# Kernel tuning notes

Measured on AMD Instinct MI355X. Metric: run time of the kernel, lower is better.

Reference implementation:

```python
import jax, jax.numpy as jnp
import numpy as np

N, E, K, IN_C, D = 50000, 800000, 3, 2, 64
RES_LAYERS = 2
EPS = 1e-5


def setup_inputs() -> dict:
    key = jax.random.key(0)
    ks = jax.random.split(key, 12)
    def w(k, shape, scale=0.05):
        return jax.random.normal(k, shape, jnp.float32) * scale
    x = jax.random.normal(ks[0], (N, IN_C), jnp.float32)
    edge_index = jax.random.randint(ks[1], (2, E), 0, N, dtype=jnp.int32)
    edge_attr = jax.random.uniform(ks[2], (E,), jnp.float32)
    # TAGConv params: first conv IN_C->D, then 2*RES_LAYERS + 1 = 5 convs D->D, each with K+1 weight mats
    tag0_w = w(ks[3], (K + 1, IN_C, D))
    tag0_b = jnp.zeros((D,), jnp.float32)
    tag_w = w(ks[4], (5, K + 1, D, D))
    tag_b = jnp.zeros((5, D), jnp.float32)
    # EdgeModel params: Lin(2D+1,D) + 2 residual blocks (Lin,ReLU,Lin)+LN + Lin(D,1)
    We0 = w(ks[5], (2 * D + 1, D)); be0 = jnp.zeros((D,), jnp.float32)
    ln0_g = jnp.ones((D,), jnp.float32); ln0_b = jnp.zeros((D,), jnp.float32)
    Wa = w(ks[6], (2, D, D)); ba = jnp.zeros((2, D), jnp.float32)
    Wb = w(ks[7], (2, D, D)); bb = jnp.zeros((2, D), jnp.float32)
    ln_g = jnp.ones((2, D), jnp.float32); ln_b = jnp.zeros((2, D), jnp.float32)
    Wf = w(ks[8], (D, 1)); bf = jnp.zeros((1,), jnp.float32)
    return dict(x=x, edge_index=edge_index, edge_attr=edge_attr,
                tag0_w=tag0_w, tag0_b=tag0_b, tag_w=tag_w, tag_b=tag_b,
                We0=We0, be0=be0, ln0_g=ln0_g, ln0_b=ln0_b,
                Wa=Wa, ba=ba, Wb=Wb, bb=bb, ln_g=ln_g, ln_b=ln_b,
                Wf=Wf, bf=bf)


def _gcn_norm(row, col, ew, n):
    # symmetric GCN normalization without self loops (PyG TAGConv default)
    deg = jnp.zeros((n,), ew.dtype).at[col].add(ew)
    deg_safe = jnp.where(deg > 0, deg, 1.0)
    dinv = jnp.where(deg > 0, jax.lax.rsqrt(deg_safe), 0.0)
    return dinv[row] * ew * dinv[col]


def _tagconv(x, row, col, norm, W, b):
    # out = sum_{k=0..K} (A_norm^k x) @ W[k] + b
    out = x @ W[0]
    h = x
    for k in range(1, K + 1):
        h = jnp.zeros(h.shape, h.dtype).at[col].add(norm[:, None] * h[row])
        out = out + h @ W[k]
    return out + b


def _inorm(x):
    # PyG InstanceNorm, single graph, affine=False: per-channel stats over nodes
    m = x.mean(0)
    v = x.var(0)
    return (x - m) * jax.lax.rsqrt(v + EPS)


def _lnorm(x, g, b):
    m = x.mean(-1, keepdims=True)
    v = x.var(-1, keepdims=True)
    return (x - m) * jax.lax.rsqrt(v + EPS) * g + b


def _forward(x, edge_index, edge_attr, tag0_w, tag0_b, tag_w, tag_b,
             We0, be0, ln0_g, ln0_b, Wa, ba, Wb, bb, ln_g, ln_b, Wf, bf):
    row, col = edge_index[0], edge_index[1]
    ew = edge_attr.reshape(-1)
    norm = _gcn_norm(row, col, ew, x.shape[0])
    # block 0: TAGConv(IN_C->D) -> InstanceNorm -> (no residual: shape change) -> ReLU
    data = jax.nn.relu(_inorm(_tagconv(x, row, col, norm, tag0_w, tag0_b)))
    # residual blocks: TAGConv -> ReLU -> TAGConv -> InstanceNorm -> +residual -> ReLU
    for i in range(RES_LAYERS):
        h = jax.nn.relu(_tagconv(data, row, col, norm, tag_w[2 * i], tag_b[2 * i]))
        h = _inorm(_tagconv(h, row, col, norm, tag_w[2 * i + 1], tag_b[2 * i + 1]))
        data = jax.nn.relu(h + data)
    # final block: TAGConv -> (no norm) -> +residual -> ReLU
    data = jax.nn.relu(_tagconv(data, row, col, norm, tag_w[4], tag_b[4]) + data)
    # edge model on gathered endpoint features + edge attr
    e = jnp.concatenate([data[row], data[col], ew[:, None]], axis=1)  # [E, 2D+1]
    h = jax.nn.relu(_lnorm(e @ We0 + be0, ln0_g, ln0_b))  # no residual (shape change)
    for j in range(2):
        h2 = jax.nn.relu(h @ Wa[j] + ba[j]) @ Wb[j] + bb[j]
        h = jax.nn.relu(_lnorm(h2, ln_g[j], ln_b[j]) + h)
    out = h @ Wf + bf  # [E, 1]
    out = (out - out.mean()) / out.std(ddof=1)
    return jnp.abs(out)


def reference(x, edge_index, edge_attr, tag0_w, tag0_b, tag_w, tag_b,
              We0, be0, ln0_g, ln0_b, Wa, ba, Wb, bb, ln_g, ln_b, Wf, bf):
    return _forward(x, edge_index, edge_attr, tag0_w, tag0_b, tag_w, tag_b,
                    We0, be0, ln0_g, ln0_b, Wa, ba, Wb, bb, ln_g, ln_b, Wf, bf)
```

## Files before the change

### kernel.cpp

```cpp
#include <hip/hip_runtime.h>

#define NN 50000
#define NE 800000
#define EPSf 1e-5f

typedef _Float16 half8 __attribute__((ext_vector_type(8)));
typedef _Float16 half4v __attribute__((ext_vector_type(4)));
typedef _Float16 half2v __attribute__((ext_vector_type(2)));
typedef float f32x4 __attribute__((ext_vector_type(4)));

#define HA_STRIDE 72
#define WB_STRIDE 72

__global__ void deg_hist_kernel(const int* __restrict__ row, const int* __restrict__ col,
                                const float* __restrict__ ew,
                                float* __restrict__ deg, int* __restrict__ cnt) {
  int e = blockIdx.x * 256 + threadIdx.x;
  if (e >= NE) return;
  int c = col[e];
  unsafeAtomicAdd(&deg[c], ew[e]);
  atomicAdd(&cnt[c], 1);
}

__global__ void dinv_kernel(float* __restrict__ deg) {
  int n = blockIdx.x * 256 + threadIdx.x;
  if (n >= NN) return;
  float d = deg[n];
  deg[n] = d > 0.f ? rsqrtf(d) : 0.f;
}

__global__ void scan1(int* __restrict__ cnt, int* __restrict__ aux) {
  __shared__ int ls[256];
  int t = threadIdx.x, idx = blockIdx.x * 256 + t;
  int v = (idx < NN) ? cnt[idx] : 0;
  ls[t] = v;
  __syncthreads();
  for (int o = 1; o < 256; o <<= 1) {
    int u = (t >= o) ? ls[t - o] : 0;
    __syncthreads();
    ls[t] += u;
    __syncthreads();
  }
  if (idx < NN) cnt[idx] = ls[t] - v;
  if (t == 255) aux[blockIdx.x] = ls[255];
}

__global__ void scan2(int* __restrict__ aux, int nb) {
  __shared__ int ls[256];
  int t = threadIdx.x;
  int v = (t < nb) ? aux[t] : 0;
  ls[t] = v;
  __syncthreads();
  for (int o = 1; o < 256; o <<= 1) {
    int u = (t >= o) ? ls[t - o] : 0;
    __syncthreads();
    ls[t] += u;
    __syncthreads();
  }
  if (t < nb) aux[t] = ls[t] - v;
}

__global__ void scan3(int* __restrict__ cnt, const int* __restrict__ aux) {
  int idx = blockIdx.x * 256 + threadIdx.x;
  if (idx < NN) cnt[idx] += aux[idx >> 8];
}

__global__ void scatter_kernel(const int* __restrict__ row, const int* __restrict__ col,
                               const float* __restrict__ ew, const float* __restrict__ dinv,
                               int* __restrict__ rowptr, int2* __restrict__ pme) {
  int e = blockIdx.x * 256 + threadIdx.x;
  if (e >= NE) return;
  int r = row[e], c = col[e];
  float w = dinv[r] * ew[e] * dinv[c];
  int p = atomicAdd(&rowptr[c], 1);
  pme[p] = make_int2(r, __float_as_int(w));
}

__global__ void cvt_w(const float* __restrict__ We0, const float* __restrict__ Wa,
                      const float* __restrict__ Wb, _Float16* __restrict__ wt) {
  int i = blockIdx.x * 256 + threadIdx.x;
  if (i < 8192) {
    int n = i >> 7, k = i & 127;
    wt[i] = (_Float16)We0[k * 64 + n];
  } else if (i < 16384) {
    int i2 = i - 8192, j = i2 >> 12, n = (i2 >> 6) & 63, k = i2 & 63;
    wt[i] = (_Float16)Wa[j * 4096 + k * 64 + n];
  } else if (i < 24576) {
    int i2 = i - 16384, j = i2 >> 12, n = (i2 >> 6) & 63, k = i2 & 63;
    wt[i] = (_Float16)Wb[j * 4096 + k * 64 + n];
  }
}

__global__ void prop16(const int* __restrict__ rowptr, const int2* __restrict__ pme,
                       const _Float16* __restrict__ h, _Float16* __restrict__ hn) {
  int idx = blockIdx.x * 256 + threadIdx.x;
  if (idx >= NN * 4) return;
  int n = idx >> 2, q = idx & 3;
  int s = n ? rowptr[n - 1] : 0;
  int epos = rowptr[n];
  const _Float16* hq = h + q * 16;
  float a[16];
#pragma unroll
  for (int i = 0; i < 16; i++) a[i] = 0.f;
  int j = s;
  for (; j + 4 <= epos; j += 4) {
    int2 m0 = pme[j], m1 = pme[j + 1], m2 = pme[j + 2], m3 = pme[j + 3];
    const half8* p0 = (const half8*)&hq[(size_t)m0.x * 64];
    const half8* p1 = (const half8*)&hq[(size_t)m1.x * 64];
    const half8* p2 = (const half8*)&hq[(size_t)m2.x * 64];
    const half8* p3 = (const half8*)&hq[(size_t)m3.x * 64];
    half8 u0 = p0[0], u1 = p0[1];
    half8 u2 = p1[0], u3 = p1[1];
    half8 u4 = p2[0], u5 = p2[1];
    half8 u6 = p3[0], u7 = p3[1];
    float w0 = __int_as_float(m0.y), w1 = __int_as_float(m1.y);
    float w2 = __int_as_float(m2.y), w3 = __int_as_float(m3.y);
#pragma unroll
    for (int i = 0; i < 8; i++) {
      a[i]     += w0 * (float)u0[i] + w1 * (float)u2[i] + w2 * (float)u4[i] + w3 * (float)u6[i];
      a[i + 8] += w0 * (float)u1[i] + w1 * (float)u3[i] + w2 * (float)u5[i] + w3 * (float)u7[i];
    }
  }
  for (; j < epos; j++) {
    int2 m = pme[j];
    float w = __int_as_float(m.y);
    const half8* p = (const half8*)&hq[(size_t)m.x * 64];
    half8 u0 = p[0], u1 = p[1];
#pragma unroll
    for (int i = 0; i < 8; i++) { a[i] += w * (float)u0[i]; a[i + 8] += w * (float)u1[i]; }
  }
  half8 o0, o1;
#pragma unroll
  for (int i = 0; i < 8; i++) { o0[i] = (_Float16)a[i]; o1[i] = (_Float16)a[i + 8]; }
  *(half8*)&hn[(size_t)n * 64 + q * 16] = o0;
  *(half8*)&hn[(size_t)n * 64 + q * 16 + 8] = o1;
}

__global__ void prop2_csr(const int* __restrict__ rowptr, const int2* __restrict__ pme,
                          const float* __restrict__ h, float* __restrict__ hn) {
  int n = blockIdx.x * 256 + threadIdx.x;
  if (n >= NN) return;
  int s = n ? rowptr[n - 1] : 0;
  int epos = rowptr[n];
  float a0 = 0.f, a1 = 0.f;
  for (int j = s; j < epos; j++) {
    int2 m = pme[j];
    float w = __int_as_float(m.y);
    a0 += w * h[m.x * 2 + 0];
    a1 += w * h[m.x * 2 + 1];
  }
  hn[n * 2 + 0] = a0;
  hn[n * 2 + 1] = a1;
}

__global__ void __launch_bounds__(128, 4) gemmB_mfma(
    const _Float16* __restrict__ h0, const _Float16* __restrict__ h1,
    const _Float16* __restrict__ h2, const _Float16* __restrict__ h3,
    const float* __restrict__ W,
    float* __restrict__ accG, const float* __restrict__ bias,
    const float* __restrict__ residF, _Float16* __restrict__ out16,
    float* __restrict__ st) {
  __shared__ __align__(16) _Float16 hA[128 * HA_STRIDE];
  __shared__ __align__(16) _Float16 WT[64 * WB_STRIDE];
  const int t = threadIdx.x;
  const int lane = t & 63, wv = t >> 6;
  const int a = lane & 15, g = lane >> 4;
  const int nb = blockIdx.x * 128;
  const _Float16* hs[4] = {h0, h1, h2, h3};

  f32x4 acc[4][4];
#pragma unroll
  for (int ct = 0; ct < 4; ct++)
#pragma unroll
    for (int nt = 0; nt < 4; nt++) acc[ct][nt] = (f32x4)0.f;

#pragma unroll 1
  for (int k = 0; k < 4; k++) {
    const _Float16* hk = hs[k];
    {
      size_t base = (size_t)(nb + t) * 64;
#pragma unroll
      for (int i = 0; i < 8; i++)
        *(half8*)&hA[t * HA_STRIDE + i * 8] = *(const half8*)&hk[base + i * 8];
    }
    {
      const float* Wk = W + k * 4096;
      int n = t >> 1, kb = (t & 1) * 32;
#pragma unroll
      for (int k2 = 0; k2 < 16; k2++) {
        int kk = kb + 2 * k2;
        half2v p = {(_Float16)Wk[kk * 64 + n], (_Float16)Wk[(kk + 1) * 64 + n]};
        *(half2v*)&WT[n * WB_STRIDE + kk] = p;
      }
    }
    __syncthreads();
#pragma unroll
    for (int ks = 0; ks < 2; ks++) {
      half8 wf[4], hf[4];
#pragma unroll
      for (int nt = 0; nt < 4; nt++)
        wf[nt] = *(const half8*)&WT[(nt * 16 + a) * WB_STRIDE + ks * 32 + g * 8];
#pragma unroll
      for (int ct = 0; ct < 4; ct++)
        hf[ct] = *(const half8*)&hA[(wv * 64 + ct * 16 + a) * HA_STRIDE + ks * 32 + g * 8];
#pragma unroll
      for (int ct = 0; ct < 4; ct++)
#pragma unroll
        for (int nt = 0; nt < 4; nt++)
          acc[ct][nt] = __builtin_amdgcn_mfma_f32_16x16x32_f16(wf[nt], hf[ct], acc[ct][nt], 0, 0, 0);
    }
    __syncthreads();
  }

  if (st) {
    f32x4 ps[4], pss[4];
#pragma unroll
    for (int nt = 0; nt < 4; nt++) { ps[nt] = (f32x4)0.f; pss[nt] = (f32x4)0.f; }
#pragma unroll
    for (int ct = 0; ct < 4; ct++) {
      int node = nb + wv * 64 + ct * 16 + a;
      if (node < NN) {
#pragma unroll
        for (int nt = 0; nt < 4; nt++) {
          ps[nt] += acc[ct][nt];
          pss[nt] += acc[ct][nt] * acc[ct][nt];
        }
      }
    }
#pragma unroll
    for (int o = 1; o < 16; o <<= 1) {
#pragma unroll
      for (int nt = 0; nt < 4; nt++)
#pragma unroll
        for (int r = 0; r < 4; r++) {
          ps[nt][r] += __shfl_xor(ps[nt][r], o);
          pss[nt][r] += __shfl_xor(pss[nt][r], o);
        }
    }
    if (a == 0) {
#pragma unroll
      for (int nt = 0; nt < 4; nt++)
#pragma unroll
        for (int r = 0; r < 4; r++) {
          unsafeAtomicAdd(&st[nt * 16 + g * 4 + r], ps[nt][r]);
          unsafeAtomicAdd(&st[64 + nt * 16 + g * 4 + r], pss[nt][r]);
        }
    }
  }

  f32x4 bias4[4];
  if (bias) {
#pragma unroll
    for (int nt = 0; nt < 4; nt++) bias4[nt] = *(const f32x4*)&bias[nt * 16 + g * 4];
  }
#pragma unroll
  for (int ct = 0; ct < 4; ct++) {
    int node = nb + wv * 64 + ct * 16 + a;
    if (node >= NN) continue;
    if (accG) {
#pragma unroll
      for (int nt = 0; nt < 4; nt++)
        *(f32x4*)&accG[(size_t)node * 64 + nt * 16 + g * 4] = acc[ct][nt];
    }
    if (out16) {
#pragma unroll
      for (int nt = 0; nt < 4; nt++) {
        f32x4 v = acc[ct][nt] + bias4[nt];
        if (residF) v += *(const f32x4*)&residF[(size_t)node * 64 + nt * 16 + g * 4];
        half4v hh = {(_Float16)fmaxf(v[0], 0.f), (_Float16)fmaxf(v[1], 0.f),
                     (_Float16)fmaxf(v[2], 0.f), (_Float16)fmaxf(v[3], 0.f)};
        *(half4v*)&out16[(size_t)node * 64 + nt * 16 + g * 4] = hh;
      }
    }
  }
}

__global__ void gemm2B(const float* __restrict__ x, const float* __restrict__ a1,
                       const float* __restrict__ a2, const float* __restrict__ a3,
                       const float* __restrict__ W,
                       float* __restrict__ acc) {
  int idx = blockIdx.x * 256 + threadIdx.x;
  if (idx >= NN * 16) return;
  int n = idx >> 4, q = idx & 15;
  const float* srcs[4] = {x, a1, a2, a3};
  float4 a = make_float4(0.f, 0.f, 0.f, 0.f);
#pragma unroll
  for (int k = 0; k < 4; k++) {
    float x0 = srcs[k][n * 2], x1 = srcs[k][n * 2 + 1];
    float4 w0 = ((const float4*)(W + k * 128))[q];
    float4 w1 = ((const float4*)(W + k * 128 + 64))[q];
    a.x += x0 * w0.x + x1 * w1.x;
    a.y += x0 * w0.y + x1 * w1.y;
    a.z += x0 * w0.z + x1 * w1.z;
    a.w += x0 * w0.w + x1 * w1.w;
  }
  ((float4*)acc)[idx] = a;
}

__global__ void stats64(const float* __restrict__ acc, float* __restrict__ st) {
  int c = threadIdx.x & 63, g = threadIdx.x >> 6;
  float s = 0.f, ss = 0.f;
  for (int n = blockIdx.x * 4 + g; n < NN; n += gridDim.x * 4) {
    float v = acc[n * 64 + c];
    s += v; ss += v * v;
  }
  __shared__ float ls[256], lss[256];
  ls[threadIdx.x] = s; lss[threadIdx.x] = ss;
  __syncthreads();
  if (threadIdx.x < 64) {
    s = ls[threadIdx.x] + ls[threadIdx.x + 64] + ls[threadIdx.x + 128] + ls[threadIdx.x + 192];
    ss = lss[threadIdx.x] + lss[threadIdx.x + 64] + lss[threadIdx.x + 128] + lss[threadIdx.x + 192];
    unsafeAtomicAdd(&st[c], s);
    unsafeAtomicAdd(&st[64 + c], ss);
  }
}

__global__ void apply64(const float* __restrict__ acc, const float* __restrict__ st,
                        const float* __restrict__ resid,
                        float* __restrict__ out32, _Float16* __restrict__ out16) {
  int idx = blockIdx.x * 256 + threadIdx.x;
  if (idx >= NN * 16) return;
  int q = idx & 15;
  int c0 = q * 4;
  const float4 av = ((const float4*)acc)[idx];
  const float invN = 1.f / NN;
  float m0 = st[c0 + 0] * invN, m1 = st[c0 + 1] * invN;
  float m2 = st[c0 + 2] * invN, m3 = st[c0 + 3] * invN;
  float r0 = rsqrtf(st[64 + c0 + 0] * invN - m0 * m0 + EPSf);
  float r1 = rsqrtf(st[64 + c0 + 1] * invN - m1 * m1 + EPSf);
  float r2 = rsqrtf(st[64 + c0 + 2] * invN - m2 * m2 + EPSf);
  float r3 = rsqrtf(st[64 + c0 + 3] * invN - m3 * m3 + EPSf);
  float v0 = (av.x - m0) * r0, v1 = (av.y - m1) * r1;
  float v2 = (av.z - m2) * r2, v3 = (av.w - m3) * r3;
  if (resid) {
    const float4 rv = ((const float4*)resid)[idx];
    v0 += rv.x; v1 += rv.y; v2 += rv.z; v3 += rv.w;
  }
  v0 = fmaxf(v0, 0.f); v1 = fmaxf(v1, 0.f);
  v2 = fmaxf(v2, 0.f); v3 = fmaxf(v3, 0.f);
  if (out32) ((float4*)out32)[idx] = make_float4(v0, v1, v2, v3);
  if (out16) {
    half4v hh = {(_Float16)v0, (_Float16)v1, (_Float16)v2, (_Float16)v3};
    *(half4v*)&out16[(size_t)idx * 4] = hh;
  }
}

__device__ __forceinline__ void gstep(f32x4 (&acc)[4][4], const _Float16* hAp,
                                      const _Float16* __restrict__ Wg, int wstride,
                                      int wv, int a, int g, int koff) {
#pragma unroll
  for (int ks = 0; ks < 2; ks++) {
    half8 wf[4], hf[4];
#pragma unroll
    for (int nt = 0; nt < 4; nt++)
      wf[nt] = *(const half8*)&Wg[(nt * 16 + a) * wstride + koff + ks * 32 + g * 8];
#pragma unroll
    for (int ct = 0; ct < 4; ct++)
      hf[ct] = *(const half8*)&hAp[(wv * 64 + ct * 16 + a) * HA_STRIDE + ks * 32 + g * 8];
#pragma unroll
    for (int ct = 0; ct < 4; ct++)
#pragma unroll
      for (int nt = 0; nt < 4; nt++)
        acc[ct][nt] = __builtin_amdgcn_mfma_f32_16x16x32_f16(wf[nt], hf[ct], acc[ct][nt], 0, 0, 0);
  }
}

__global__ void __launch_bounds__(256, 2) edge_mlp_mfma(
    const _Float16* __restrict__ dat16, const int* __restrict__ row, const int* __restrict__ col,
    const float* __restrict__ ew, const _Float16* __restrict__ wt16,
    const float* __restrict__ We0, const float* __restrict__ be0,
    const float* __restrict__ g0, const float* __restrict__ b0,
    const float* __restrict__ ba, const float* __restrict__ bb,
    const float* __restrict__ lg, const float* __restrict__ lb,
    const float* __restrict__ Wf, const float* __restrict__ bfp,
    float* __restrict__ eout) {
  __shared__ __align__(16) _Float16 hA[256 * HA_STRIDE];
  const _Float16* wt0 = wt16;
  const _Float16* wtA = wt16 + 8192;
  const _Float16* wtB = wt16 + 16384;

  const int t = threadIdx.x;
  const int lane = t & 63, wv = t >> 6;
  const int a = lane & 15, g = lane >> 4;
  const int eb = blockIdx.x * 256;

  {
    int e = eb + t;
    int r = row[e];
    const _Float16* srcp = dat16 + (size_t)r * 64;
#pragma unroll
    for (int i = 0; i < 8; i++)
      *(half8*)&hA[t * HA_STRIDE + i * 8] = *(const half8*)&srcp[i * 8];
  }

  f32x4 be0v[4], w128v[4], g0v[4], b0v[4];
#pragma unroll
  for (int nt = 0; nt < 4; nt++) {
    int ch = nt * 16 + g * 4;
    be0v[nt] = *(const f32x4*)&be0[ch];
    w128v[nt] = *(const f32x4*)&We0[128 * 64 + ch];
    g0v[nt] = *(const f32x4*)&g0[ch];
    b0v[nt] = *(const f32x4*)&b0[ch];
  }

  f32x4 acc[4][4];
#pragma unroll
  for (int ct = 0; ct < 4; ct++) {
    float we = ew[eb + wv * 64 + ct * 16 + a];
#pragma unroll
    for (int nt = 0; nt < 4; nt++) acc[ct][nt] = be0v[nt] + we * w128v[nt];
  }
  __syncthreads();
  gstep(acc, hA, wt0, 128, wv, a, g, 0);
  __syncthreads();
  {
    int e = eb + t;
    int c = col[e];
    const _Float16* srcp = dat16 + (size_t)c * 64;
#pragma unroll
    for (int i = 0; i < 8; i++)
      *(half8*)&hA[t * HA_STRIDE + i * 8] = *(const half8*)&srcp[i * 8];
  }
  __syncthreads();
  gstep(acc, hA, wt0, 128, wv, a, g, 64);

  f32x4 h[4][4];
#pragma unroll
  for (int ct = 0; ct < 4; ct++) {
    float s = 0.f, ss = 0.f;
#pragma unroll
    for (int nt = 0; nt < 4; nt++)
#pragma unroll
      for (int r = 0; r < 4; r++) { float v = acc[ct][nt][r]; s += v; ss += v * v; }
    s += __shfl_xor(s, 16); ss += __shfl_xor(ss, 16);
    s += __shfl_xor(s, 32); ss += __shfl_xor(ss, 32);
    float m = s * (1.f / 64);
    float is = rsqrtf(ss * (1.f / 64) - m * m + EPSf);
#pragma unroll
    for (int nt = 0; nt < 4; nt++)
#pragma unroll
      for (int r = 0; r < 4; r++)
        h[ct][nt][r] = fmaxf((acc[ct][nt][r] - m) * is * g0v[nt][r] + b0v[nt][r], 0.f);
  }
  __syncthreads();

#pragma unroll 1
  for (int j = 0; j < 2; j++) {
#pragma unroll
    for (int ct = 0; ct < 4; ct++)
#pragma unroll
      for (int nt = 0; nt < 4; nt++) {
        half4v hh = {(_Float16)h[ct][nt][0], (_Float16)h[ct][nt][1],
                     (_Float16)h[ct][nt][2], (_Float16)h[ct][nt][3]};
        *(half4v*)&hA[(wv * 64 + ct * 16 + a) * HA_STRIDE + nt * 16 + g * 4] = hh;
      }
    __syncthreads();
    f32x4 accT[4][4];
#pragma unroll
    for (int nt = 0; nt < 4; nt++) {
      f32x4 bv = *(const f32x4*)&ba[j * 64 + nt * 16 + g * 4];
#pragma unroll
      for (int ct = 0; ct < 4; ct++) accT[ct][nt] = bv;
    }
    gstep(accT, hA, wtA + j * 4096, 64, wv, a, g, 0);
    __syncthreads();
#pragma unroll
    for (int ct = 0; ct < 4; ct++)
#pragma unroll
      for (int nt = 0; nt < 4; nt++) {
        half4v hh = {(_Float16)fmaxf(accT[ct][nt][0], 0.f), (_Float16)fmaxf(accT[ct][nt][1], 0.f),
                     (_Float16)fmaxf(accT[ct][nt][2], 0.f), (_Float16)fmaxf(accT[ct][nt][3], 0.f)};
        *(half4v*)&hA[(wv * 64 + ct * 16 + a) * HA_STRIDE + nt * 16 + g * 4] = hh;
      }
    __syncthreads();
    f32x4 accB[4][4];
#pragma unroll
    for (int nt = 0; nt < 4; nt++) {
      f32x4 bv = *(const f32x4*)&bb[j * 64 + nt * 16 + g * 4];
#pragma unroll
      for (int ct = 0; ct < 4; ct++) accB[ct][nt] = bv;
    }
    gstep(accB, hA, wtB + j * 4096, 64, wv, a, g, 0);

    f32x4 lgv[4], lbv[4];
#pragma unroll
    for (int nt = 0; nt < 4; nt++) {
      lgv[nt] = *(const f32x4*)&lg[j * 64 + nt * 16 + g * 4];
      lbv[nt] = *(const f32x4*)&lb[j * 64 + nt * 16 + g * 4];
    }
#pragma unroll
    for (int ct = 0; ct < 4; ct++) {
      float s = 0.f, ss = 0.f;
#pragma unroll
      for (int nt = 0; nt < 4; nt++)
#pragma unroll
        for (int r = 0; r < 4; r++) { float v = accB[ct][nt][r]; s += v; ss += v * v; }
      s += __shfl_xor(s, 16); ss += __shfl_xor(ss, 16);
      s += __shfl_xor(s, 32); ss += __shfl_xor(ss, 32);
      float m = s * (1.f / 64);
      float is = rsqrtf(ss * (1.f / 64) - m * m + EPSf);
#pragma unroll
      for (int nt = 0; nt < 4; nt++)
#pragma unroll
        for (int r = 0; r < 4; r++)
          h[ct][nt][r] =
              fmaxf((accB[ct][nt][r] - m) * is * lgv[nt][r] + lbv[nt][r] + h[ct][nt][r], 0.f);
    }
    __syncthreads();
  }

  f32x4 wfv[4];
#pragma unroll
  for (int nt = 0; nt < 4; nt++) wfv[nt] = *(const f32x4*)&Wf[nt * 16 + g * 4];
  float p0 = 0.f, p1 = 0.f, p2 = 0.f, p3 = 0.f;
#pragma unroll
  for (int nt = 0; nt < 4; nt++)
#pragma unroll
    for (int r = 0; r < 4; r++) {
      p0 += h[0][nt][r] * wfv[nt][r];
      p1 += h[1][nt][r] * wfv[nt][r];
      p2 += h[2][nt][r] * wfv[nt][r];
      p3 += h[3][nt][r] * wfv[nt][r];
    }
  p0 += __shfl_xor(p0, 16); p0 += __shfl_xor(p0, 32);
  p1 += __shfl_xor(p1, 16); p1 += __shfl_xor(p1, 32);
  p2 += __shfl_xor(p2, 16); p2 += __shfl_xor(p2, 32);
  p3 += __shfl_xor(p3, 16); p3 += __shfl_xor(p3, 32);
  float sel = (g == 0) ? p0 : (g == 1) ? p1 : (g == 2) ? p2 : p3;
  eout[eb + t] = sel + bfp[0];
}

__global__ void reduce2(const float* __restrict__ v, float* __restrict__ est) {
  __shared__ float ls[256], lss[256];
  float s = 0.f, ss = 0.f;
  for (int i = blockIdx.x * 256 + threadIdx.x; i < NE; i += gridDim.x * 256) {
    float a = v[i]; s += a; ss += a * a;
  }
  ls[threadIdx.x] = s; lss[threadIdx.x] = ss;
  __syncthreads();
  for (int o = 128; o > 0; o >>= 1) {
    if (threadIdx.x < o) { ls[threadIdx.x] += ls[threadIdx.x + o]; lss[threadIdx.x] += lss[threadIdx.x + o]; }
    __syncthreads();
  }
  if (threadIdx.x == 0) {
    unsafeAtomicAdd(&est[0], ls[0]);
    unsafeAtomicAdd(&est[1], lss[0]);
  }
}

__global__ void finalize(const float* __restrict__ eo, const float* __restrict__ est,
                         float* __restrict__ out) {
  int e = blockIdx.x * 256 + threadIdx.x;
  if (e >= NE) return;
  float sum = est[0], ssq = est[1];
  float m = sum * (1.f / NE);
  float var = (ssq - sum * sum * (1.f / NE)) * (1.f / (NE - 1));
  out[e] = fabsf((eo[e] - m) * rsqrtf(var));
}

extern "C" void kernel_launch(void* const* d_in, const int* in_sizes, int n_in,
                              void* d_out, int out_size, void* d_ws, size_t ws_size,
                              hipStream_t stream) {
  const float* x   = (const float*)d_in[0];
  const int*   ei  = (const int*)d_in[1];
  const float* ew  = (const float*)d_in[2];
  const float* t0w = (const float*)d_in[3];
  const float* t0b = (const float*)d_in[4];
  const float* tw  = (const float*)d_in[5];
  const float* tb  = (const float*)d_in[6];
  const float* We0 = (const float*)d_in[7];
  const float* be0 = (const float*)d_in[8];
  const float* g0  = (const float*)d_in[9];
  const float* b0  = (const float*)d_in[10];
  const float* Wa  = (const float*)d_in[11];
  const float* ba  = (const float*)d_in[12];
  const float* Wb  = (const float*)d_in[13];
  const float* bb  = (const float*)d_in[14];
  const float* lg  = (const float*)d_in[15];
  const float* lb  = (const float*)d_in[16];
  const float* Wf  = (const float*)d_in[17];
  const float* bf  = (const float*)d_in[18];
  const int* row = ei;
  const int* col = ei + NE;
  (void)t0b;

  float* ws = (float*)d_ws;
  int*       rowptr = (int*)ws;
  int2*      pme    = (int2*)(ws + 50048);
  float*     st     = ws + 1650048;
  float*     est    = st + 128;
  float*     acc    = ws + 1650240;
  float*     dat    = acc + 3200000;
  _Float16*  cur16  = (_Float16*)(ws + 8050240);
  _Float16*  mid16  = (_Float16*)(ws + 9650240);
  _Float16*  h1     = (_Float16*)(ws + 11250240);
  _Float16*  h2     = (_Float16*)(ws + 12850240);
  _Float16*  h3     = (_Float16*)(ws + 14450240);
  float*     eout   = ws + 16050240;
  _Float16*  wt16   = (_Float16*)(ws + 16850240);
  float*     dinv   = ws + 11250240;
  int*       aux    = (int*)(ws + 12850240);
  float*     b2a    = ws + 14450240;
  float*     b2b    = b2a + 100096;
  float*     b2c    = b2b + 100096;

  dim3 blk(256);
#define GRID(n) dim3(((n) + 255) / 256)
  const int NB = (NN + 255) / 256;

  hipMemsetAsync(dinv, 0, NN * sizeof(float), stream);
  hipMemsetAsync(rowptr, 0, NN * sizeof(int), stream);
  deg_hist_kernel<<<GRID(NE), blk, 0, stream>>>(row, col, ew, dinv, rowptr);
  dinv_kernel<<<GRID(NN), blk, 0, stream>>>(dinv);
  scan1<<<dim3(NB), blk, 0, stream>>>(rowptr, aux);
  scan2<<<dim3(1), blk, 0, stream>>>(aux, NB);
  scan3<<<dim3(NB), blk, 0, stream>>>(rowptr, aux);
  scatter_kernel<<<GRID(NE), blk, 0, stream>>>(row, col, ew, dinv, rowptr, pme);
  cvt_w<<<dim3(96), blk, 0, stream>>>(We0, Wa, Wb, wt16);

  prop2_csr<<<dim3(NB), blk, 0, stream>>>(rowptr, pme, x, b2a);
  prop2_csr<<<dim3(NB), blk, 0, stream>>>(rowptr, pme, b2a, b2b);
  prop2_csr<<<dim3(NB), blk, 0, stream>>>(rowptr, pme, b2b, b2c);
  gemm2B<<<GRID(NN * 16), blk, 0, stream>>>(x, b2a, b2b, b2c, t0w, acc);
  hipMemsetAsync(st, 0, 128 * sizeof(float), stream);
  stats64<<<dim3(128), blk, 0, stream>>>(acc, st);
  apply64<<<GRID(NN * 16), blk, 0, stream>>>(acc, st, nullptr, dat, cur16);

  const int GBB = (NN + 127) / 128;
  auto props = [&](const _Float16* src) {
    prop16<<<GRID(NN * 4), blk, 0, stream>>>(rowptr, pme, src, h1);
    prop16<<<GRID(NN * 4), blk, 0, stream>>>(rowptr, pme, h1, h2);
    prop16<<<GRID(NN * 4), blk, 0, stream>>>(rowptr, pme, h2, h3);
  };

  for (int i = 0; i < 2; i++) {
    props(cur16);
    gemmB_mfma<<<dim3(GBB), dim3(128), 0, stream>>>(
        cur16, h1, h2, h3, tw + (2 * i) * 16384,
        nullptr, tb + (2 * i) * 64, nullptr, mid16, nullptr);
    props(mid16);
    hipMemsetAsync(st, 0, 128 * sizeof(float), stream);
    gemmB_mfma<<<dim3(GBB), dim3(128), 0, stream>>>(
        mid16, h1, h2, h3, tw + (2 * i + 1) * 16384,
        acc, nullptr, nullptr, nullptr, st);
    apply64<<<GRID(NN * 16), blk, 0, stream>>>(acc, st, dat, dat, cur16);
  }
  props(cur16);
  gemmB_mfma<<<dim3(GBB), dim3(128), 0, stream>>>(
      cur16, h1, h2, h3, tw + 4 * 16384,
      nullptr, tb + 4 * 64, dat, cur16, nullptr);

  edge_mlp_mfma<<<GRID(NE), blk, 0, stream>>>(cur16, row, col, ew, wt16, We0, be0, g0, b0,
                                              ba, bb, lg, lb, Wf, bf, eout);
  hipMemsetAsync(est, 0, 2 * sizeof(float), stream);
  reduce2<<<dim3(1024), blk, 0, stream>>>(eout, est);
  finalize<<<GRID(NE), blk, 0, stream>>>(eout, est, (float*)d_out);
#undef GRID
}
```

Measured before the change: 920.7 us.

## Pre-transpose TAGConv weights to fp16, widen prop16 threading, stage edge-MLP weights in LDS

Converts and transposes all TAGConv weight matrices to fp16 once in cvt_w, so gemmB_mfma loads them with vectorized half8 copies instead of strided fp32 reads and per-element conversion. prop16 now uses 8 threads per node with 8 channels each instead of 4 threads with 16, which raises parallelism and cuts per-thread registers for the gather. edge_mlp_mfma stages each weight matrix into a shared-memory tile before every MFMA step rather than reading weight fragments from global memory, and its launch bounds go from 2 to 3 blocks per CU. The extra LDS tile and the occupancy target may squeeze registers, and narrower prop16 threads issue more index and weight loads per channel.

```diff
diff --git a/kernel.cpp b/kernel.cpp
--- a/kernel.cpp
+++ b/kernel.cpp
@@ -6,7 +6,6 @@
 
 typedef _Float16 half8 __attribute__((ext_vector_type(8)));
 typedef _Float16 half4v __attribute__((ext_vector_type(4)));
-typedef _Float16 half2v __attribute__((ext_vector_type(2)));
 typedef float f32x4 __attribute__((ext_vector_type(4)));
 
 #define HA_STRIDE 72
@@ -77,7 +76,8 @@
 }
 
 __global__ void cvt_w(const float* __restrict__ We0, const float* __restrict__ Wa,
-                      const float* __restrict__ Wb, _Float16* __restrict__ wt) {
+                      const float* __restrict__ Wb, const float* __restrict__ tw,
+                      _Float16* __restrict__ wt) {
   int i = blockIdx.x * 256 + threadIdx.x;
   if (i < 8192) {
     int n = i >> 7, k = i & 127;
@@ -88,52 +88,48 @@
   } else if (i < 24576) {
     int i2 = i - 16384, j = i2 >> 12, n = (i2 >> 6) & 63, k = i2 & 63;
     wt[i] = (_Float16)Wb[j * 4096 + k * 64 + n];
+  } else if (i < 106496) {
+    int i2 = i - 24576;
+    int p = i2 >> 12, n = (i2 >> 6) & 63, kk = i2 & 63;
+    wt[i] = (_Float16)tw[p * 4096 + kk * 64 + n];
   }
 }
 
 __global__ void prop16(const int* __restrict__ rowptr, const int2* __restrict__ pme,
                        const _Float16* __restrict__ h, _Float16* __restrict__ hn) {
   int idx = blockIdx.x * 256 + threadIdx.x;
-  if (idx >= NN * 4) return;
-  int n = idx >> 2, q = idx & 3;
+  if (idx >= NN * 8) return;
+  int n = idx >> 3, q = idx & 7;
   int s = n ? rowptr[n - 1] : 0;
   int epos = rowptr[n];
-  const _Float16* hq = h + q * 16;
-  float a[16];
-#pragma unroll
-  for (int i = 0; i < 16; i++) a[i] = 0.f;
+  const _Float16* hq = h + q * 8;
+  float a[8];
+#pragma unroll
+  for (int i = 0; i < 8; i++) a[i] = 0.f;
   int j = s;
   for (; j + 4 <= epos; j += 4) {
     int2 m0 = pme[j], m1 = pme[j + 1], m2 = pme[j + 2], m3 = pme[j + 3];
-    const half8* p0 = (const half8*)&hq[(size_t)m0.x * 64];
-    const half8* p1 = (const half8*)&hq[(size_t)m1.x * 64];
-    const half8* p2 = (const half8*)&hq[(size_t)m2.x * 64];
-    const half8* p3 = (const half8*)&hq[(size_t)m3.x * 64];
-    half8 u0 = p0[0], u1 = p0[1];
-    half8 u2 = p1[0], u3 = p1[1];
-    half8 u4 = p2[0], u5 = p2[1];
-    half8 u6 = p3[0], u7 = p3[1];
+    half8 u0 = *(const half8*)&hq[(size_t)m0.x * 64];
+    half8 u1 = *(const half8*)&hq[(size_t)m1.x * 64];
+    half8 u2 = *(const half8*)&hq[(size_t)m2.x * 64];
+    half8 u3 = *(const half8*)&hq[(size_t)m3.x * 64];
     float w0 = __int_as_float(m0.y), w1 = __int_as_float(m1.y);
     float w2 = __int_as_float(m2.y), w3 = __int_as_float(m3.y);
 #pragma unroll
-    for (int i = 0; i < 8; i++) {
-      a[i]     += w0 * (float)u0[i] + w1 * (float)u2[i] + w2 * (float)u4[i] + w3 * (float)u6[i];
-      a[i + 8] += w0 * (float)u1[i] + w1 * (float)u3[i] + w2 * (float)u5[i] + w3 * (float)u7[i];
-    }
+    for (int i = 0; i < 8; i++)
+      a[i] += w0 * (float)u0[i] + w1 * (float)u1[i] + w2 * (float)u2[i] + w3 * (float)u3[i];
   }
   for (; j < epos; j++) {
     int2 m = pme[j];
     float w = __int_as_float(m.y);
-    const half8* p = (const half8*)&hq[(size_t)m.x * 64];
-    half8 u0 = p[0], u1 = p[1];
-#pragma unroll
-    for (int i = 0; i < 8; i++) { a[i] += w * (float)u0[i]; a[i + 8] += w * (float)u1[i]; }
-  }
-  half8 o0, o1;
-#pragma unroll
-  for (int i = 0; i < 8; i++) { o0[i] = (_Float16)a[i]; o1[i] = (_Float16)a[i + 8]; }
-  *(half8*)&hn[(size_t)n * 64 + q * 16] = o0;
-  *(half8*)&hn[(size_t)n * 64 + q * 16 + 8] = o1;
+    half8 u = *(const half8*)&hq[(size_t)m.x * 64];
+#pragma unroll
+    for (int i = 0; i < 8; i++) a[i] += w * (float)u[i];
+  }
+  half8 o;
+#pragma unroll
+  for (int i = 0; i < 8; i++) o[i] = (_Float16)a[i];
+  *(half8*)&hn[(size_t)n * 64 + q * 8] = o;
 }
 
 __global__ void prop2_csr(const int* __restrict__ rowptr, const int2* __restrict__ pme,
@@ -156,7 +152,7 @@
 __global__ void __launch_bounds__(128, 4) gemmB_mfma(
     const _Float16* __restrict__ h0, const _Float16* __restrict__ h1,
     const _Float16* __restrict__ h2, const _Float16* __restrict__ h3,
-    const float* __restrict__ W,
+    const _Float16* __restrict__ WT16,
     float* __restrict__ accG, const float* __restrict__ bias,
     const float* __restrict__ residF, _Float16* __restrict__ out16,
     float* __restrict__ st) {
@@ -184,14 +180,11 @@
         *(half8*)&hA[t * HA_STRIDE + i * 8] = *(const half8*)&hk[base + i * 8];
     }
     {
-      const float* Wk = W + k * 4096;
-      int n = t >> 1, kb = (t & 1) * 32;
-#pragma unroll
-      for (int k2 = 0; k2 < 16; k2++) {
-        int kk = kb + 2 * k2;
-        half2v p = {(_Float16)Wk[kk * 64 + n], (_Float16)Wk[(kk + 1) * 64 + n]};
-        *(half2v*)&WT[n * WB_STRIDE + kk] = p;
-      }
+      const _Float16* Wk = WT16 + k * 4096;
+      int n = t >> 1, c0 = (t & 1) * 32;
+#pragma unroll
+      for (int u = 0; u < 4; u++)
+        *(half8*)&WT[n * WB_STRIDE + c0 + u * 8] = *(const half8*)&Wk[n * 64 + c0 + u * 8];
     }
     __syncthreads();
 #pragma unroll
@@ -277,8 +270,7 @@
 
 __global__ void gemm2B(const float* __restrict__ x, const float* __restrict__ a1,
                        const float* __restrict__ a2, const float* __restrict__ a3,
-                       const float* __restrict__ W,
-                       float* __restrict__ acc) {
+                       const float* __restrict__ W, float* __restrict__ acc) {
   int idx = blockIdx.x * 256 + threadIdx.x;
   if (idx >= NN * 16) return;
   int n = idx >> 4, q = idx & 15;
@@ -346,14 +338,13 @@
 }
 
 __device__ __forceinline__ void gstep(f32x4 (&acc)[4][4], const _Float16* hAp,
-                                      const _Float16* __restrict__ Wg, int wstride,
-                                      int wv, int a, int g, int koff) {
+                                      const _Float16* WTp, int wv, int a, int g) {
 #pragma unroll
   for (int ks = 0; ks < 2; ks++) {
     half8 wf[4], hf[4];
 #pragma unroll
     for (int nt = 0; nt < 4; nt++)
-      wf[nt] = *(const half8*)&Wg[(nt * 16 + a) * wstride + koff + ks * 32 + g * 8];
+      wf[nt] = *(const half8*)&WTp[(nt * 16 + a) * WB_STRIDE + ks * 32 + g * 8];
 #pragma unroll
     for (int ct = 0; ct < 4; ct++)
       hf[ct] = *(const half8*)&hAp[(wv * 64 + ct * 16 + a) * HA_STRIDE + ks * 32 + g * 8];
@@ -365,7 +356,7 @@
   }
 }
 
-__global__ void __launch_bounds__(256, 2) edge_mlp_mfma(
+__global__ void __launch_bounds__(256, 3) edge_mlp_mfma(
     const _Float16* __restrict__ dat16, const int* __restrict__ row, const int* __restrict__ col,
     const float* __restrict__ ew, const _Float16* __restrict__ wt16,
     const float* __restrict__ We0, const float* __restrict__ be0,
@@ -375,6 +366,7 @@
     const float* __restrict__ Wf, const float* __restrict__ bfp,
     float* __restrict__ eout) {
   __shared__ __align__(16) _Float16 hA[256 * HA_STRIDE];
+  __shared__ __align__(16) _Float16 WT[64 * WB_STRIDE];
   const _Float16* wt0 = wt16;
   const _Float16* wtA = wt16 + 8192;
   const _Float16* wtB = wt16 + 16384;
@@ -384,14 +376,20 @@
   const int a = lane & 15, g = lane >> 4;
   const int eb = blockIdx.x * 256;
 
-  {
-    int e = eb + t;
-    int r = row[e];
-    const _Float16* srcp = dat16 + (size_t)r * 64;
+  auto stageW = [&](const _Float16* src, int stride, int koff) {
+    int n = t >> 2, c0 = (t & 3) * 16;
+    *(half8*)&WT[n * WB_STRIDE + c0] = *(const half8*)&src[n * stride + koff + c0];
+    *(half8*)&WT[n * WB_STRIDE + c0 + 8] = *(const half8*)&src[n * stride + koff + c0 + 8];
+  };
+  auto stageH = [&](int node) {
+    const _Float16* srcp = dat16 + (size_t)node * 64;
 #pragma unroll
     for (int i = 0; i < 8; i++)
       *(half8*)&hA[t * HA_STRIDE + i * 8] = *(const half8*)&srcp[i * 8];
-  }
+  };
+
+  stageH(row[eb + t]);
+  stageW(wt0, 128, 0);
 
   f32x4 be0v[4], w128v[4], g0v[4], b0v[4];
 #pragma unroll
@@ -411,18 +409,12 @@
     for (int nt = 0; nt < 4; nt++) acc[ct][nt] = be0v[nt] + we * w128v[nt];
   }
   __syncthreads();
-  gstep(acc, hA, wt0, 128, wv, a, g, 0);
-  __syncthreads();
-  {
-    int e = eb + t;
-    int c = col[e];
-    const _Float16* srcp = dat16 + (size_t)c * 64;
-#pragma unroll
-    for (int i = 0; i < 8; i++)
-      *(half8*)&hA[t * HA_STRIDE + i * 8] = *(const half8*)&srcp[i * 8];
-  }
-  __syncthreads();
-  gstep(acc, hA, wt0, 128, wv, a, g, 64);
+  gstep(acc, hA, WT, wv, a, g);
+  __syncthreads();
+  stageH(col[eb + t]);
+  stageW(wt0, 128, 64);
+  __syncthreads();
+  gstep(acc, hA, WT, wv, a, g);
 
   f32x4 h[4][4];
 #pragma unroll
@@ -454,6 +446,7 @@
                      (_Float16)h[ct][nt][2], (_Float16)h[ct][nt][3]};
         *(half4v*)&hA[(wv * 64 + ct * 16 + a) * HA_STRIDE + nt * 16 + g * 4] = hh;
       }
+    stageW(wtA + j * 4096, 64, 0);
     __syncthreads();
     f32x4 accT[4][4];
 #pragma unroll
@@ -462,7 +455,7 @@
 #pragma unroll
       for (int ct = 0; ct < 4; ct++) accT[ct][nt] = bv;
     }
-    gstep(accT, hA, wtA + j * 4096, 64, wv, a, g, 0);
+    gstep(accT, hA, WT, wv, a, g);
     __syncthreads();
 #pragma unroll
     for (int ct = 0; ct < 4; ct++)
@@ -472,6 +465,7 @@
                      (_Float16)fmaxf(accT[ct][nt][2], 0.f), (_Float16)fmaxf(accT[ct][nt][3], 0.f)};
         *(half4v*)&hA[(wv * 64 + ct * 16 + a) * HA_STRIDE + nt * 16 + g * 4] = hh;
       }
+    stageW(wtB + j * 4096, 64, 0);
     __syncthreads();
     f32x4 accB[4][4];
 #pragma unroll
@@ -480,7 +474,7 @@
 #pragma unroll
       for (int ct = 0; ct < 4; ct++) accB[ct][nt] = bv;
     }
-    gstep(accB, hA, wtB + j * 4096, 64, wv, a, g, 0);
+    gstep(accB, hA, WT, wv, a, g);
 
     f32x4 lgv[4], lbv[4];
 #pragma unroll
@@ -565,7 +559,6 @@
   const int*   ei  = (const int*)d_in[1];
   const float* ew  = (const float*)d_in[2];
   const float* t0w = (const float*)d_in[3];
-  const float* t0b = (const float*)d_in[4];
   const float* tw  = (const float*)d_in[5];
   const float* tb  = (const float*)d_in[6];
   const float* We0 = (const float*)d_in[7];
@@ -582,7 +575,6 @@
   const float* bf  = (const float*)d_in[18];
   const int* row = ei;
   const int* col = ei + NE;
-  (void)t0b;
 
   float* ws = (float*)d_ws;
   int*       rowptr = (int*)ws;
@@ -603,6 +595,7 @@
   float*     b2a    = ws + 14450240;
   float*     b2b    = b2a + 100096;
   float*     b2c    = b2b + 100096;
+  _Float16*  wtT    = wt16 + 24576;
 
   dim3 blk(256);
 #define GRID(n) dim3(((n) + 255) / 256)
@@ -616,7 +609,7 @@
   scan2<<<dim3(1), blk, 0, stream>>>(aux, NB);
   scan3<<<dim3(NB), blk, 0, stream>>>(rowptr, aux);
   scatter_kernel<<<GRID(NE), blk, 0, stream>>>(row, col, ew, dinv, rowptr, pme);
-  cvt_w<<<dim3(96), blk, 0, stream>>>(We0, Wa, Wb, wt16);
+  cvt_w<<<dim3(416), blk, 0, stream>>>(We0, Wa, Wb, tw, wt16);
 
   prop2_csr<<<dim3(NB), blk, 0, stream>>>(rowptr, pme, x, b2a);
   prop2_csr<<<dim3(NB), blk, 0, stream>>>(rowptr, pme, b2a, b2b);
@@ -628,26 +621,26 @@
 
   const int GBB = (NN + 127) / 128;
   auto props = [&](const _Float16* src) {
-    prop16<<<GRID(NN * 4), blk, 0, stream>>>(rowptr, pme, src, h1);
-    prop16<<<GRID(NN * 4), blk, 0, stream>>>(rowptr, pme, h1, h2);
-    prop16<<<GRID(NN * 4), blk, 0, stream>>>(rowptr, pme, h2, h3);
+    prop16<<<GRID(NN * 8), blk, 0, stream>>>(rowptr, pme, src, h1);
+    prop16<<<GRID(NN * 8), blk, 0, stream>>>(rowptr, pme, h1, h2);
+    prop16<<<GRID(NN * 8), blk, 0, stream>>>(rowptr, pme, h2, h3);
   };
 
   for (int i = 0; i < 2; i++) {
     props(cur16);
     gemmB_mfma<<<dim3(GBB), dim3(128), 0, stream>>>(
-        cur16, h1, h2, h3, tw + (2 * i) * 16384,
+        cur16, h1, h2, h3, wtT + (2 * i) * 16384,
         nullptr, tb + (2 * i) * 64, nullptr, mid16, nullptr);
     props(mid16);
     hipMemsetAsync(st, 0, 128 * sizeof(float), stream);
     gemmB_mfma<<<dim3(GBB), dim3(128), 0, stream>>>(
-        mid16, h1, h2, h3, tw + (2 * i + 1) * 16384,
+        mid16, h1, h2, h3, wtT + (2 * i + 1) * 16384,
         acc, nullptr, nullptr, nullptr, st);
     apply64<<<GRID(NN * 16), blk, 0, stream>>>(acc, st, dat, dat, cur16);
   }
   props(cur16);
   gemmB_mfma<<<dim3(GBB), dim3(128), 0, stream>>>(
-      cur16, h1, h2, h3, tw + 4 * 16384,
+      cur16, h1, h2, h3, wtT + 4 * 16384,
       nullptr, tb + 4 * 64, dat, cur16, nullptr);
 
   edge_mlp_mfma<<<GRID(NE), blk, 0, stream>>>(cur16, row, col, ew, wt16, We0, be0, g0, b0,
```

Result: faster. 842.5 us (-8.5%).
